# Kernel tuning notes

Measured on AMD Instinct MI355X. Metric: run time of the kernel, lower is better.

## Reference

```python
import jax, jax.numpy as jnp
import numpy as np

LN_EPS = 1e-5      # torch nn.LayerNorm default
NORM_EPS = 1e-12   # torch F.normalize default
EPS = 1e-8         # loss eps


def layer_norm(x, gamma, beta):
    mu = x.mean(axis=-1, keepdims=True)
    var = x.var(axis=-1, keepdims=True)  # biased, matches torch LN
    return (x - mu) * jax.lax.rsqrt(var + LN_EPS) * gamma + beta


def l2norm(x):
    n = jnp.sqrt(jnp.sum(x * x, axis=-1, keepdims=True))
    return x / jnp.maximum(n, NORM_EPS)


def setup_inputs() -> dict:
    key = jax.random.key(0)
    k1, k2, k3 = jax.random.split(key, 3)
    N, B, L, D = 1024, 64, 197, 768
    text_features = jax.random.normal(k1, (N, D), dtype=jnp.float32)
    vision_tokens = jax.random.normal(k2, (B, L, D), dtype=jnp.float32)
    group_map = jnp.sort(jax.random.randint(k3, (N,), 0, B)).astype(jnp.int64)
    ln_gamma = jnp.ones((D,), dtype=jnp.float32)
    ln_beta = jnp.zeros((D,), dtype=jnp.float32)
    log_loss_temp = jnp.array([np.log(0.07)], dtype=jnp.float32)
    return {
        "text_features": text_features,
        "vision_tokens": vision_tokens,
        "group_map": group_map,
        "ln_gamma": ln_gamma,
        "ln_beta": ln_beta,
        "log_loss_temp": log_loss_temp,
    }


def reference(text_features, vision_tokens, group_map, ln_gamma, ln_beta, log_loss_temp):
    D = text_features.shape[-1]
    # shared LayerNorm on both modalities
    tf = layer_norm(text_features, ln_gamma, ln_beta)          # [N, D]
    vt = layer_norm(vision_tokens, ln_gamma, ln_beta)          # [B, L, D]

    # SimilarityLogit, sim_op='dot': scores / sqrt(D), softmax over tokens
    scores = jnp.einsum('nd,bld->bnl', tf, vt) / jnp.sqrt(jnp.float32(D))
    attn = jax.nn.softmax(scores, axis=-1)                     # [B, N, L]
    aggregated = jnp.einsum('bnl,bld->bnd', attn, vt)          # [B, N, D]

    qn = l2norm(tf)                                            # [N, D]
    an = l2norm(aggregated)                                    # [B, N, D]
    logits = jnp.einsum('nd,bnd->nb', qn, an)                  # [N, B] (== [B,N].T)

    # multi-positive NCE loss (row_sum=False, col_sum=False)
    temp = jnp.exp(log_loss_temp)[0]
    scaled = jnp.exp(logits / temp)                            # [N, B]
    N = scaled.shape[0]
    idx = jnp.arange(N)
    pos = scaled[idx, group_map]                               # [N]

    # row loss: pos / sum over images
    row_p = pos / (scaled.sum(axis=1) + EPS)
    row_loss = -jnp.log(row_p + EPS)

    # column loss: pos / (pos + sum of negatives in its column)
    neg_mask = jnp.ones_like(scaled).at[idx, group_map].set(0.0)
    sum_neg = (scaled * neg_mask).sum(axis=0)[group_map]       # [N]
    col_p = pos / (pos + sum_neg + EPS)
    col_loss = -jnp.log(col_p + EPS)

    return (row_loss.mean() + col_loss.mean()) / 2
```

## Files before the change

### kernel.cpp

```cpp
#include <hip/hip_runtime.h>
#include <hip/hip_bf16.h>
#include <math.h>

#define NN 1024
#define BB 64
#define LL 197
#define LP 256
#define DD 768

typedef __attribute__((ext_vector_type(8))) short short8;
typedef __attribute__((ext_vector_type(4))) float f32x4;

constexpr float LN_EPS = 1e-5f;
constexpr float NORM_EPS = 1e-12f;
constexpr float EPS = 1e-8f;

__device__ __forceinline__ float waveSum(float v) {
#pragma unroll
    for (int m = 32; m >= 1; m >>= 1) v += __shfl_xor(v, m, 64);
    return v;
}
__device__ __forceinline__ float grpSum(float v) {
#pragma unroll
    for (int m = 8; m >= 1; m >>= 1) v += __shfl_xor(v, m, 64);
    return v;
}
__device__ __forceinline__ float grpMax(float v) {
#pragma unroll
    for (int m = 8; m >= 1; m >>= 1) v = fmaxf(v, __shfl_xor(v, m, 64));
    return v;
}

__device__ __forceinline__ float bf2f(unsigned short u) {
    unsigned int x = ((unsigned int)u) << 16;
    return reinterpret_cast<float&>(x);
}

__device__ __forceinline__ void gl_lds16(const void* g, void* l) {
    __builtin_amdgcn_global_load_lds(
        (const __attribute__((address_space(1))) unsigned int*)g,
        (__attribute__((address_space(3))) unsigned int*)l, 16, 0, 0);
}

__global__ __launch_bounds__(256) void ln_kernel(
    const float* __restrict__ x, __hip_bfloat16* __restrict__ y,
    const float* __restrict__ gamma, const float* __restrict__ beta,
    float* __restrict__ qinv) {
    const int row = blockIdx.x;
    const int tid = threadIdx.x;
    const float* xr = x + (size_t)row * DD;
    __hip_bfloat16* yr = y + (size_t)row * DD;

    float v[3];
    float s = 0.f, ss = 0.f;
#pragma unroll
    for (int c = 0; c < 3; c++) {
        float t = xr[tid + 256 * c];
        v[c] = t; s += t; ss += t * t;
    }
    __shared__ float red[8];
    s = waveSum(s); ss = waveSum(ss);
    const int w = tid >> 6;
    if ((tid & 63) == 0) { red[w] = s; red[4 + w] = ss; }
    __syncthreads();
    s = red[0] + red[1] + red[2] + red[3];
    ss = red[4] + red[5] + red[6] + red[7];
    const float mean = s * (1.f / DD);
    const float var = ss * (1.f / DD) - mean * mean;
    const float rs = rsqrtf(var + LN_EPS);

    float q = 0.f;
#pragma unroll
    for (int c = 0; c < 3; c++) {
        const int d = tid + 256 * c;
        float t = (v[c] - mean) * rs * gamma[d] + beta[d];
        __hip_bfloat16 hb = __float2bfloat16(t);
        yr[d] = hb;
        float tb = __bfloat162float(hb);
        q += tb * tb;
    }
    __syncthreads();
    q = waveSum(q);
    if ((tid & 63) == 0) red[w] = q;
    __syncthreads();
    if (tid == 0) {
        float n2 = red[0] + red[1] + red[2] + red[3];
        qinv[row] = 1.f / fmaxf(sqrtf(n2), NORM_EPS);
    }
}

__global__ __launch_bounds__(256) void ln_vis_kernel(
    const float* __restrict__ x, __hip_bfloat16* __restrict__ y,
    const float* __restrict__ gamma, const float* __restrict__ beta) {
    const int id = blockIdx.x;
    const int xcd = id & 7;
    const int k = id >> 3;
    const int bhi = k >> 8;
    const int l = k & 255;
    const int b = xcd + 8 * bhi;
    const int tid = threadIdx.x;
    __hip_bfloat16* yr = y + ((size_t)b * LP + l) * DD;
    if (l >= LL) {
#pragma unroll
        for (int c = 0; c < 3; c++) yr[tid + 256 * c] = __float2bfloat16(0.f);
        return;
    }
    const float* xr = x + ((size_t)b * LL + l) * DD;

    float v[3];
    float s = 0.f, ss = 0.f;
#pragma unroll
    for (int c = 0; c < 3; c++) {
        float t = xr[tid + 256 * c];
        v[c] = t; s += t; ss += t * t;
    }
    __shared__ float red[8];
    s = waveSum(s); ss = waveSum(ss);
    const int w = tid >> 6;
    if ((tid & 63) == 0) { red[w] = s; red[4 + w] = ss; }
    __syncthreads();
    s = red[0] + red[1] + red[2] + red[3];
    ss = red[4] + red[5] + red[6] + red[7];
    const float mean = s * (1.f / DD);
    const float var = ss * (1.f / DD) - mean * mean;
    const float rs = rsqrtf(var + LN_EPS);
#pragma unroll
    for (int c = 0; c < 3; c++) {
        const int d = tid + 256 * c;
        yr[d] = __float2bfloat16((v[c] - mean) * rs * gamma[d] + beta[d]);
    }
}

__global__ __launch_bounds__(256, 2) void gram_kernel(
    const __hip_bfloat16* __restrict__ vt, __hip_bfloat16* __restrict__ G) {
    const int id = blockIdx.x;
    const int xcd = id & 7;
    const int k = id >> 3;
    const int bhi = k >> 3;
    const int rb = k & 7;
    const int b = xcd + 8 * bhi;
    const int n0 = rb * 32;
    const int tid = threadIdx.x, w = tid >> 6, lane = tid & 63;
    const int g = lane >> 4, c = lane & 15;
    const int gsw = (g ^ ((c ^ (c >> 2)) & 3)) * 16;

    __shared__ __align__(16) unsigned char smem[55296];
    const char* vtbc = (const char*)(vt + (size_t)b * LP * DD);

#define GSTAGE(ks, bsel)                                                        \
    {                                                                           \
        const int kb_ = (ks) * 64;                                              \
        _Pragma("unroll")                                                       \
        for (int q_ = 0; q_ < 4; q_++) {                                        \
            const int o_ = q_ * 4096 + tid * 16;                                \
            const int r_ = o_ >> 6;                                             \
            const int sj_ = ((o_ >> 4) & 3) ^ ((r_ ^ (r_ >> 2)) & 3);           \
            gl_lds16(vtbc + (size_t)r_ * 1536 + kb_ + sj_ * 16,                 \
                     smem + (bsel) * 16384 + q_ * 4096 + w * 1024);             \
        }                                                                       \
        if (w < 2) {                                                            \
            const int o_ = tid * 16;                                            \
            const int r_ = o_ >> 6;                                             \
            const int sj_ = ((o_ >> 4) & 3) ^ ((r_ ^ (r_ >> 2)) & 3);           \
            gl_lds16(vtbc + (size_t)(n0 + r_) * 1536 + kb_ + sj_ * 16,          \
                     smem + 49152 + (bsel) * 2048 + w * 1024);                  \
        }                                                                       \
    }

    f32x4 acc[4][2];
#pragma unroll
    for (int i = 0; i < 4; i++)
#pragma unroll
        for (int nb = 0; nb < 2; nb++) acc[i][nb] = {0.f, 0.f, 0.f, 0.f};

    GSTAGE(0, 0);
    GSTAGE(1, 1);
    asm volatile("s_waitcnt vmcnt(4)" ::: "memory");
    __syncthreads();

    for (int ks = 0; ks < 24; ks++) {
        if (ks < 22) GSTAGE(ks + 2, (ks + 2) % 3);
        const unsigned char* vb = smem + (ks % 3) * 16384;
        const unsigned char* tb = smem + 49152 + (ks % 3) * 2048;
        short8 af[2], bf[4];
#pragma unroll
        for (int nb = 0; nb < 2; nb++)
            af[nb] = *(const short8*)(tb + (nb * 16 + c) * 64 + gsw);
#pragma unroll
        for (int i = 0; i < 4; i++)
            bf[i] = *(const short8*)(vb + ((w + 4 * i) * 16 + c) * 64 + gsw);
#pragma unroll
        for (int i = 0; i < 4; i++)
#pragma unroll
            for (int nb = 0; nb < 2; nb++)
                acc[i][nb] = __builtin_amdgcn_mfma_f32_16x16x32_bf16(
                    af[nb], bf[i], acc[i][nb], 0, 0, 0);
        if (ks < 22) asm volatile("s_waitcnt vmcnt(4)" ::: "memory");
        else         asm volatile("s_waitcnt vmcnt(0)" ::: "memory");
        __syncthreads();
    }
#undef GSTAGE

    __hip_bfloat16* Gb = G + (size_t)b * LP * LP;
#pragma unroll
    for (int i = 0; i < 4; i++) {
        const int col = (w + 4 * i) * 16 + c;
#pragma unroll
        for (int nb = 0; nb < 2; nb++)
#pragma unroll
            for (int r = 0; r < 4; r++)
                Gb[(size_t)(n0 + nb * 16 + g * 4 + r) * LP + col] =
                    __float2bfloat16(acc[i][nb][r]);
    }
}

__global__ __launch_bounds__(256, 3) void score_kernel(
    const __hip_bfloat16* __restrict__ tf, const __hip_bfloat16* __restrict__ vt,
    const float* __restrict__ qinv, __hip_bfloat16* __restrict__ Pbuf,
    float* __restrict__ numq) {
    const int id = blockIdx.x;
    const int xcd = id & 7;
    const int kk = id >> 3;
    const int bhi = kk >> 4;
    const int nt = kk & 15;
    const int b = xcd + 8 * bhi;
    const int n0 = nt * 64;
    const int tid = threadIdx.x, w = tid >> 6, lane = tid & 63;
    const int g = lane >> 4, c = lane & 15;
    const int gsw = (g ^ ((c ^ (c >> 2)) & 3)) * 16;

    __shared__ __align__(16) unsigned char smem[61440];
    float* mx = (float*)smem;
    float* sm = mx + 256;
    float* nm = sm + 256;

    const char* vtbc = (const char*)(vt + (size_t)b * LP * DD);
    const char* tfc = (const char*)(tf + (size_t)n0 * DD);

#define SSTAGE(ks, bsel)                                                        \
    {                                                                           \
        const int kb_ = (ks) * 64;                                              \
        _Pragma("unroll")                                                       \
        for (int q_ = 0; q_ < 4; q_++) {                                        \
            const int o_ = q_ * 4096 + tid * 16;                                \
            const int r_ = o_ >> 6;                                             \
            const int sj_ = ((o_ >> 4) & 3) ^ ((r_ ^ (r_ >> 2)) & 3);           \
            gl_lds16(vtbc + (size_t)r_ * 1536 + kb_ + sj_ * 16,                 \
                     smem + (bsel) * 16384 + q_ * 4096 + w * 1024);             \
        }                                                                       \
        {                                                                       \
            const int o_ = tid * 16;                                            \
            const int r_ = o_ >> 6;                                             \
            const int sj_ = ((o_ >> 4) & 3) ^ ((r_ ^ (r_ >> 2)) & 3);           \
            gl_lds16(tfc + (size_t)r_ * 1536 + kb_ + sj_ * 16,                  \
                     smem + 49152 + (bsel) * 4096 + w * 1024);                  \
        }                                                                       \
    }

    f32x4 acc[4][4];
#pragma unroll
    for (int i = 0; i < 4; i++)
#pragma unroll
        for (int nb = 0; nb < 4; nb++) acc[i][nb] = {0.f, 0.f, 0.f, 0.f};

    SSTAGE(0, 0);
    SSTAGE(1, 1);
    asm volatile("s_waitcnt vmcnt(5)" ::: "memory");
    __syncthreads();

    for (int ks = 0; ks < 24; ks++) {
        if (ks < 22) SSTAGE(ks + 2, (ks + 2) % 3);
        const unsigned char* vb = smem + (ks % 3) * 16384;
        const unsigned char* tb = smem + 49152 + (ks % 3) * 4096;
        short8 af[4], bf[4];
#pragma unroll
        for (int nb = 0; nb < 4; nb++)
            af[nb] = *(const short8*)(tb + (nb * 16 + c) * 64 + gsw);
#pragma unroll
        for (int i = 0; i < 4; i++)
            bf[i] = *(const short8*)(vb + ((w + 4 * i) * 16 + c) * 64 + gsw);
#pragma unroll
        for (int i = 0; i < 4; i++)
#pragma unroll
            for (int nb = 0; nb < 4; nb++)
                acc[i][nb] = __builtin_amdgcn_mfma_f32_16x16x32_bf16(
                    af[nb], bf[i], acc[i][nb], 0, 0, 0);
        if (ks < 22) asm volatile("s_waitcnt vmcnt(5)" ::: "memory");
        else         asm volatile("s_waitcnt vmcnt(0)" ::: "memory");
        __syncthreads();
    }
#undef SSTAGE

    const float inv_sqrtD = 0.0360843918f;
    float mp[4][4];
#pragma unroll
    for (int nb = 0; nb < 4; nb++)
#pragma unroll
        for (int r = 0; r < 4; r++) mp[nb][r] = -1e30f;
#pragma unroll
    for (int i = 0; i < 4; i++) {
        const int l = (w + 4 * i) * 16 + c;
        if (l < LL) {
#pragma unroll
            for (int nb = 0; nb < 4; nb++)
#pragma unroll
                for (int r = 0; r < 4; r++) mp[nb][r] = fmaxf(mp[nb][r], acc[i][nb][r]);
        }
    }
#pragma unroll
    for (int nb = 0; nb < 4; nb++)
#pragma unroll
        for (int r = 0; r < 4; r++) mp[nb][r] = grpMax(mp[nb][r]);
    if (c == 0) {
#pragma unroll
        for (int nb = 0; nb < 4; nb++)
#pragma unroll
            for (int r = 0; r < 4; r++) mx[(nb * 16 + g * 4 + r) * 4 + w] = mp[nb][r];
    }
    __syncthreads();
    float mf[4][4];
#pragma unroll
    for (int nb = 0; nb < 4; nb++)
#pragma unroll
        for (int r = 0; r < 4; r++) {
            const int row = nb * 16 + g * 4 + r;
            mf[nb][r] = fmaxf(fmaxf(mx[row * 4 + 0], mx[row * 4 + 1]),
                              fmaxf(mx[row * 4 + 2], mx[row * 4 + 3]));
        }

    float sp[4][4], np[4][4];
#pragma unroll
    for (int nb = 0; nb < 4; nb++)
#pragma unroll
        for (int r = 0; r < 4; r++) { sp[nb][r] = 0.f; np[nb][r] = 0.f; }
#pragma unroll
    for (int i = 0; i < 4; i++) {
        const int l = (w + 4 * i) * 16 + c;
#pragma unroll
        for (int nb = 0; nb < 4; nb++)
#pragma unroll
            for (int r = 0; r < 4; r++) {
                const float raw = acc[i][nb][r];
                const float p = (l < LL) ? __expf((raw - mf[nb][r]) * inv_sqrtD) : 0.f;
                acc[i][nb][r] = p;
                sp[nb][r] += p;
                np[nb][r] += p * raw;
            }
    }
#pragma unroll
    for (int nb = 0; nb < 4; nb++)
#pragma unroll
        for (int r = 0; r < 4; r++) { sp[nb][r] = grpSum(sp[nb][r]); np[nb][r] = grpSum(np[nb][r]); }
    if (c == 0) {
#pragma unroll
        for (int nb = 0; nb < 4; nb++)
#pragma unroll
            for (int r = 0; r < 4; r++) {
                const int row = nb * 16 + g * 4 + r;
                sm[row * 4 + w] = sp[nb][r];
                nm[row * 4 + w] = np[nb][r];
            }
    }
    __syncthreads();

    float invs[4][4];
#pragma unroll
    for (int nb = 0; nb < 4; nb++)
#pragma unroll
        for (int r = 0; r < 4; r++) {
            const int row = nb * 16 + g * 4 + r;
            const float ssum = sm[row * 4 + 0] + sm[row * 4 + 1] + sm[row * 4 + 2] + sm[row * 4 + 3];
            invs[nb][r] = 1.f / ssum;
        }

    __hip_bfloat16* Pb = Pbuf + ((size_t)b * NN + n0) * LP;
#pragma unroll
    for (int i = 0; i < 4; i++) {
        const int lb = w + 4 * i;
#pragma unroll
        for (int nb = 0; nb < 4; nb++)
#pragma unroll
            for (int r = 0; r < 4; r++)
                Pb[(size_t)(nb * 16 + g * 4 + r) * LP + lb * 16 + c] =
                    __float2bfloat16(acc[i][nb][r] * invs[nb][r]);
    }

    if (tid < 64) {
        const int row = tid;
        const int n = n0 + row;
        const float ssum = sm[row * 4 + 0] + sm[row * 4 + 1] + sm[row * 4 + 2] + sm[row * 4 + 3];
        const float nsum = nm[row * 4 + 0] + nm[row * 4 + 1] + nm[row * 4 + 2] + nm[row * 4 + 3];
        numq[(size_t)n * BB + b] = (nsum / ssum) * qinv[n];
    }
}

__global__ __launch_bounds__(256, 3) void den_kernel(
    const __hip_bfloat16* __restrict__ Pbuf, const __hip_bfloat16* __restrict__ G,
    const float* __restrict__ numq, float* __restrict__ logits) {
    const int id = blockIdx.x;
    const int xcd = id & 7;
    const int kk = id >> 3;
    const int bhi = kk >> 4;
    const int nt = kk & 15;
    const int b = xcd + 8 * bhi;
    const int n0 = nt * 64;
    const int tid = threadIdx.x, w = tid >> 6, lane = tid & 63;
    const int g = lane >> 4, c = lane & 15;
    const int gsw = (g ^ ((c ^ (c >> 2)) & 3)) * 16;

    __shared__ __align__(16) unsigned char smem[61440];
    float* mx = (float*)smem;

    const char* Gbc = (const char*)(G + (size_t)b * LP * LP);
    const char* Pbc = (const char*)(Pbuf + ((size_t)b * NN + n0) * LP);

#define DSTAGE(ks, bsel)                                                        \
    {                                                                           \
        const int kb_ = (ks) * 64;                                              \
        _Pragma("unroll")                                                       \
        for (int q_ = 0; q_ < 4; q_++) {                                        \
            const int o_ = q_ * 4096 + tid * 16;                                \
            const int r_ = o_ >> 6;                                             \
            const int sj_ = ((o_ >> 4) & 3) ^ ((r_ ^ (r_ >> 2)) & 3);           \
            gl_lds16(Gbc + (size_t)r_ * 512 + kb_ + sj_ * 16,                   \
                     smem + (bsel) * 16384 + q_ * 4096 + w * 1024);             \
        }                                                                       \
        {                                                                       \
            const int o_ = tid * 16;                                            \
            const int r_ = o_ >> 6;                                             \
            const int sj_ = ((o_ >> 4) & 3) ^ ((r_ ^ (r_ >> 2)) & 3);           \
            gl_lds16(Pbc + (size_t)r_ * 512 + kb_ + sj_ * 16,                   \
                     smem + 49152 + (bsel) * 4096 + w * 1024);                  \
        }                                                                       \
    }

    f32x4 acc[4][4];
#pragma unroll
    for (int i = 0; i < 4; i++)
#pragma unroll
        for (int nb = 0; nb < 4; nb++) acc[i][nb] = {0.f, 0.f, 0.f, 0.f};

    DSTAGE(0, 0);
    DSTAGE(1, 1);
    asm volatile("s_waitcnt vmcnt(5)" ::: "memory");
    __syncthreads();

    for (int ks = 0; ks < 8; ks++) {
        if (ks < 6) DSTAGE(ks + 2, (ks + 2) % 3);
        const unsigned char* vb = smem + (ks % 3) * 16384;
        const unsigned char* tb = smem + 49152 + (ks % 3) * 4096;
        short8 af[4], bf[4];
#pragma unroll
        for (int nb = 0; nb < 4; nb++)
            af[nb] = *(const short8*)(tb + (nb * 16 + c) * 64 + gsw);
#pragma unroll
        for (int i = 0; i < 4; i++)
            bf[i] = *(const short8*)(vb + ((w + 4 * i) * 16 + c) * 64 + gsw);
#pragma unroll
        for (int i = 0; i < 4; i++)
#pragma unroll
            for (int nb = 0; nb < 4; nb++)
                acc[i][nb] = __builtin_amdgcn_mfma_f32_16x16x32_bf16(
                    af[nb], bf[i], acc[i][nb], 0, 0, 0);
        if (ks < 6) asm volatile("s_waitcnt vmcnt(5)" ::: "memory");
        else        asm volatile("s_waitcnt vmcnt(0)" ::: "memory");
        __syncthreads();
    }
#undef DSTAGE

    const short* Pb = (const short*)Pbc;
    float den[4][4];
#pragma unroll
    for (int nb = 0; nb < 4; nb++)
#pragma unroll
        for (int r = 0; r < 4; r++) den[nb][r] = 0.f;
#pragma unroll
    for (int i = 0; i < 4; i++) {
        const int col = (w + 4 * i) * 16 + c;
#pragma unroll
        for (int nb = 0; nb < 4; nb++)
#pragma unroll
            for (int r = 0; r < 4; r++) {
                const float P = bf2f((unsigned short)Pb[(size_t)(nb * 16 + g * 4 + r) * LP + col]);
                den[nb][r] += P * acc[i][nb][r];
            }
    }

#pragma unroll
    for (int nb = 0; nb < 4; nb++)
#pragma unroll
        for (int r = 0; r < 4; r++) den[nb][r] = grpSum(den[nb][r]);
    if (c == 0) {
#pragma unroll
        for (int nb = 0; nb < 4; nb++)
#pragma unroll
            for (int r = 0; r < 4; r++) mx[(nb * 16 + g * 4 + r) * 4 + w] = den[nb][r];
    }
    __syncthreads();
    if (tid < 64) {
        const int row = tid;
        const int n = n0 + row;
        const float dsum = mx[row * 4 + 0] + mx[row * 4 + 1] + mx[row * 4 + 2] + mx[row * 4 + 3];
        const float dn = fmaxf(sqrtf(fmaxf(dsum, 0.f)), NORM_EPS);
        logits[(size_t)n * BB + b] = numq[(size_t)n * BB + b] / dn;
    }
}

__global__ __launch_bounds__(64) void loss_row_kernel(
    const float* __restrict__ logits, const int* __restrict__ gm,
    const float* __restrict__ logtemp, float* __restrict__ scaled,
    float* __restrict__ posv, float* __restrict__ rowloss) {
    const int n = blockIdx.x;
    const int b = threadIdx.x;
    const float invtemp = 1.f / expf(logtemp[0]);
    const float e = expf(logits[(size_t)n * BB + b] * invtemp);
    scaled[(size_t)n * BB + b] = e;
    const float sum = waveSum(e);
    const int g = gm[n];
    const float pos = __shfl(e, g, 64);
    if (b == 0) {
        posv[n] = pos;
        rowloss[n] = -logf(pos / (sum + EPS) + EPS);
    }
}

__global__ __launch_bounds__(256) void colsum_kernel(
    const float* __restrict__ scaled, const int* __restrict__ gm,
    float* __restrict__ colsum, float* __restrict__ poscol) {
    const int b = blockIdx.x;
    const int tid = threadIdx.x;
    float s = 0.f, p = 0.f;
    for (int n = tid; n < NN; n += 256) {
        const float e = scaled[(size_t)n * BB + b];
        s += e;
        if (gm[n] == b) p += e;
    }
    s = waveSum(s); p = waveSum(p);
    __shared__ float red[8];
    const int w = tid >> 6;
    if ((tid & 63) == 0) { red[w] = s; red[4 + w] = p; }
    __syncthreads();
    if (tid == 0) {
        colsum[b] = red[0] + red[1] + red[2] + red[3];
        poscol[b] = red[4] + red[5] + red[6] + red[7];
    }
}

__global__ __launch_bounds__(1024) void final_kernel(
    const float* __restrict__ posv, const float* __restrict__ rowloss,
    const float* __restrict__ colsum, const float* __restrict__ poscol,
    const int* __restrict__ gm, float* __restrict__ out) {
    const int n = threadIdx.x;
    const int g = gm[n];
    const float pos = posv[n];
    const float sum_neg = colsum[g] - poscol[g];
    const float cl = -logf(pos / (pos + sum_neg + EPS) + EPS);
    float v = rowloss[n] + cl;
    v = waveSum(v);
    __shared__ float red[16];
    if ((n & 63) == 0) red[n >> 6] = v;
    __syncthreads();
    if (n == 0) {
        float s = 0.f;
#pragma unroll
        for (int i = 0; i < 16; i++) s += red[i];
        out[0] = s / (2.f * NN);
    }
}

extern "C" void kernel_launch(void* const* d_in, const int* in_sizes, int n_in,
                              void* d_out, int out_size, void* d_ws, size_t ws_size,
                              hipStream_t stream) {
    const float* text = (const float*)d_in[0];
    const float* vis = (const float*)d_in[1];
    const int* gm = (const int*)d_in[2];
    const float* gamma = (const float*)d_in[3];
    const float* beta = (const float*)d_in[4];
    const float* logtemp = (const float*)d_in[5];
    float* out = (float*)d_out;

    char* w = (char*)d_ws;
    __hip_bfloat16* tf = (__hip_bfloat16*)w;             w += (size_t)NN * DD * 2;
    __hip_bfloat16* vt = (__hip_bfloat16*)w;             w += (size_t)BB * LP * DD * 2;
    __hip_bfloat16* G  = (__hip_bfloat16*)w;             w += (size_t)BB * LP * LP * 2;
    __hip_bfloat16* Pbuf = (__hip_bfloat16*)w;           w += (size_t)BB * NN * LP * 2;
    float* qinv    = (float*)w;  w += (size_t)NN * 4;
    float* numq    = (float*)w;  w += (size_t)NN * BB * 4;
    float* logits  = (float*)w;  w += (size_t)NN * BB * 4;
    float* scaled  = (float*)w;  w += (size_t)NN * BB * 4;
    float* posv    = (float*)w;  w += (size_t)NN * 4;
    float* rowloss = (float*)w;  w += (size_t)NN * 4;
    float* colsum  = (float*)w;  w += (size_t)BB * 4;
    float* poscol  = (float*)w;  w += (size_t)BB * 4;

    ln_kernel<<<NN, 256, 0, stream>>>(text, tf, gamma, beta, qinv);
    ln_vis_kernel<<<BB * LP, 256, 0, stream>>>(vis, vt, gamma, beta);

    score_kernel<<<1024, 256, 0, stream>>>(tf, vt, qinv, Pbuf, numq);
    gram_kernel<<<512, 256, 0, stream>>>(vt, G);
    den_kernel<<<1024, 256, 0, stream>>>(Pbuf, G, numq, logits);

    loss_row_kernel<<<NN, 64, 0, stream>>>(logits, gm, logtemp, scaled, posv, rowloss);
    colsum_kernel<<<BB, 256, 0, stream>>>(scaled, gm, colsum, poscol);
    final_kernel<<<1, 1024, 0, stream>>>(posv, rowloss, colsum, poscol, gm, out);
}
```

Before: 123.1 us.

## Switch score/denom GEMMs to double-buffered LDS and use raw barriers

```diff
diff --git a/kernel.cpp b/kernel.cpp
--- a/kernel.cpp
+++ b/kernel.cpp
@@ -40,6 +40,12 @@
     __builtin_amdgcn_global_load_lds(
         (const __attribute__((address_space(1))) unsigned int*)g,
         (__attribute__((address_space(3))) unsigned int*)l, 16, 0, 0);
+}
+
+__device__ __forceinline__ void raw_barrier() {
+    __builtin_amdgcn_sched_barrier(0);
+    __builtin_amdgcn_s_barrier();
+    __builtin_amdgcn_sched_barrier(0);
 }
 
 __global__ __launch_bounds__(256) void ln_kernel(
@@ -176,7 +182,7 @@
     GSTAGE(0, 0);
     GSTAGE(1, 1);
     asm volatile("s_waitcnt vmcnt(4)" ::: "memory");
-    __syncthreads();
+    raw_barrier();
 
     for (int ks = 0; ks < 24; ks++) {
         if (ks < 22) GSTAGE(ks + 2, (ks + 2) % 3);
@@ -195,9 +201,10 @@
             for (int nb = 0; nb < 2; nb++)
                 acc[i][nb] = __builtin_amdgcn_mfma_f32_16x16x32_bf16(
                     af[nb], bf[i], acc[i][nb], 0, 0, 0);
+        __builtin_amdgcn_sched_barrier(0);
         if (ks < 22) asm volatile("s_waitcnt vmcnt(4)" ::: "memory");
         else         asm volatile("s_waitcnt vmcnt(0)" ::: "memory");
-        __syncthreads();
+        raw_barrier();
     }
 #undef GSTAGE
 
@@ -229,7 +236,7 @@
     const int g = lane >> 4, c = lane & 15;
     const int gsw = (g ^ ((c ^ (c >> 2)) & 3)) * 16;
 
-    __shared__ __align__(16) unsigned char smem[61440];
+    __shared__ __align__(16) unsigned char smem[40960];
     float* mx = (float*)smem;
     float* sm = mx + 256;
     float* nm = sm + 256;
@@ -253,7 +260,7 @@
             const int r_ = o_ >> 6;                                             \
             const int sj_ = ((o_ >> 4) & 3) ^ ((r_ ^ (r_ >> 2)) & 3);           \
             gl_lds16(tfc + (size_t)r_ * 1536 + kb_ + sj_ * 16,                  \
-                     smem + 49152 + (bsel) * 4096 + w * 1024);                  \
+                     smem + 32768 + (bsel) * 4096 + w * 1024);                  \
         }                                                                       \
     }
 
@@ -266,12 +273,11 @@
     SSTAGE(0, 0);
     SSTAGE(1, 1);
     asm volatile("s_waitcnt vmcnt(5)" ::: "memory");
-    __syncthreads();
+    raw_barrier();
 
     for (int ks = 0; ks < 24; ks++) {
-        if (ks < 22) SSTAGE(ks + 2, (ks + 2) % 3);
-        const unsigned char* vb = smem + (ks % 3) * 16384;
-        const unsigned char* tb = smem + 49152 + (ks % 3) * 4096;
+        const unsigned char* vb = smem + (ks & 1) * 16384;
+        const unsigned char* tb = smem + 32768 + (ks & 1) * 4096;
         short8 af[4], bf[4];
 #pragma unroll
         for (int nb = 0; nb < 4; nb++)
@@ -285,9 +291,14 @@
             for (int nb = 0; nb < 4; nb++)
                 acc[i][nb] = __builtin_amdgcn_mfma_f32_16x16x32_bf16(
                     af[nb], bf[i], acc[i][nb], 0, 0, 0);
-        if (ks < 22) asm volatile("s_waitcnt vmcnt(5)" ::: "memory");
-        else         asm volatile("s_waitcnt vmcnt(0)" ::: "memory");
-        __syncthreads();
+        raw_barrier();
+        if (ks < 22) {
+            SSTAGE(ks + 2, ks & 1);
+            asm volatile("s_waitcnt vmcnt(5)" ::: "memory");
+        } else {
+            asm volatile("s_waitcnt vmcnt(0)" ::: "memory");
+        }
+        raw_barrier();
     }
 #undef SSTAGE
 
@@ -408,7 +419,7 @@
     const int g = lane >> 4, c = lane & 15;
     const int gsw = (g ^ ((c ^ (c >> 2)) & 3)) * 16;
 
-    __shared__ __align__(16) unsigned char smem[61440];
+    __shared__ __align__(16) unsigned char smem[40960];
     float* mx = (float*)smem;
 
     const char* Gbc = (const char*)(G + (size_t)b * LP * LP);
@@ -430,7 +441,7 @@
             const int r_ = o_ >> 6;                                             \
             const int sj_ = ((o_ >> 4) & 3) ^ ((r_ ^ (r_ >> 2)) & 3);           \
             gl_lds16(Pbc + (size_t)r_ * 512 + kb_ + sj_ * 16,                   \
-                     smem + 49152 + (bsel) * 4096 + w * 1024);                  \
+                     smem + 32768 + (bsel) * 4096 + w * 1024);                  \
         }                                                                       \
     }
 
@@ -443,12 +454,11 @@
     DSTAGE(0, 0);
     DSTAGE(1, 1);
     asm volatile("s_waitcnt vmcnt(5)" ::: "memory");
-    __syncthreads();
+    raw_barrier();
 
     for (int ks = 0; ks < 8; ks++) {
-        if (ks < 6) DSTAGE(ks + 2, (ks + 2) % 3);
-        const unsigned char* vb = smem + (ks % 3) * 16384;
-        const unsigned char* tb = smem + 49152 + (ks % 3) * 4096;
+        const unsigned char* vb = smem + (ks & 1) * 16384;
+        const unsigned char* tb = smem + 32768 + (ks & 1) * 4096;
         short8 af[4], bf[4];
 #pragma unroll
         for (int nb = 0; nb < 4; nb++)
@@ -462,9 +472,14 @@
             for (int nb = 0; nb < 4; nb++)
                 acc[i][nb] = __builtin_amdgcn_mfma_f32_16x16x32_bf16(
                     af[nb], bf[i], acc[i][nb], 0, 0, 0);
-        if (ks < 6) asm volatile("s_waitcnt vmcnt(5)" ::: "memory");
-        else        asm volatile("s_waitcnt vmcnt(0)" ::: "memory");
-        __syncthreads();
+        raw_barrier();
+        if (ks < 6) {
+            DSTAGE(ks + 2, ks & 1);
+            asm volatile("s_waitcnt vmcnt(5)" ::: "memory");
+        } else {
+            asm volatile("s_waitcnt vmcnt(0)" ::: "memory");
+        }
+        raw_barrier();
     }
 #undef DSTAGE
 
@@ -490,6 +505,7 @@
     for (int nb = 0; nb < 4; nb++)
 #pragma unroll
         for (int r = 0; r < 4; r++) den[nb][r] = grpSum(den[nb][r]);
+    __syncthreads();
     if (c == 0) {
 #pragma unroll
         for (int nb = 0; nb < 4; nb++)
```

New measurement: 119.1 us. 3.3% less time.
